# Kernel tuning notes

Hardware: AMD Instinct MI355X
Metric: run time of the kernel (lower is better)

The kernel has to match this reference:

```python
import math
import jax, jax.numpy as jnp
import numpy as np

H = 16  # num_heads
B, L, D = 1, 256, 1024


def setup_inputs() -> dict:
    key = jax.random.key(0)
    ks = jax.random.split(key, 12)
    s = 1.0 / math.sqrt(D)  # keep activations O(1)
    inp = {
        "mu": jax.random.normal(ks[0], (B, L, D), jnp.float32),
        "var": jax.random.uniform(ks[1], (B, L, D), jnp.float32) + 0.1,
    }
    names = ["q_mu", "q_var", "k_mu", "k_var", "v_mu", "v_var", "o_mu", "o_var"]
    for i, n in enumerate(names):
        inp["w" + n] = jax.random.normal(ks[2 + i], (D, D), jnp.float32) * s
        inp["b" + n] = jnp.zeros((D,), jnp.float32)
    return inp


def _split_heads(x):
    b, l, d = x.shape
    return x.reshape(b, l, H, d // H).transpose(0, 2, 1, 3)  # [B,H,L,Dh]


def _combine_heads(x):
    b, h, l, dh = x.shape
    return x.transpose(0, 2, 1, 3).reshape(b, l, h * dh)


def reference(mu, var, wq_mu, bq_mu, wq_var, bq_var, wk_mu, bk_mu, wk_var, bk_var,
              wv_mu, bv_mu, wv_var, bv_var, wo_mu, bo_mu, wo_var, bo_var):
    dk = mu.shape[-1] // H
    Qm = _split_heads(mu @ wq_mu + bq_mu)
    Qv = _split_heads(jax.nn.softplus(var @ wq_var + bq_var))
    Km = _split_heads(mu @ wk_mu + bk_mu)
    Kv = _split_heads(jax.nn.softplus(var @ wk_var + bk_var))
    Vm = _split_heads(mu @ wv_mu + bv_mu)
    Vv = _split_heads(jax.nn.softplus(var @ wv_var + bv_var))

    # per-element Gaussian KL, broadcast to [B,H,Lq,Lk,Dh] (as in the original)
    diff = (Qm[:, :, :, None, :] - Km[:, :, None, :, :]) ** 2
    ratio = Qv[:, :, :, None, :] / Kv[:, :, None, :, :]
    kl = diff / (2.0 * Kv[:, :, None, :, :]) + 0.5 * (ratio - jnp.log(ratio) - 1.0)
    scores = -kl.sum(-1) * (1.0 / math.sqrt(dk))  # [B,H,Lq,Lk]
    attn = jax.nn.softmax(scores, axis=-1)

    out_mu = jnp.einsum("bhqk,bhkd->bhqd", attn, Vm)
    out_var = jnp.einsum("bhqk,bhkd->bhqd", attn ** 2, Vv)

    O_mu = _combine_heads(out_mu)
    O_var = _combine_heads(out_var)
    mu_out = O_mu @ wo_mu + bo_mu
    var_out = jax.nn.softplus(O_var @ wo_var + bo_var)
    return mu_out, var_out
```

## Files before the change

### kernel.cpp

```cpp
#include <hip/hip_runtime.h>
#include <math.h>

typedef __bf16 bf16_t;
typedef bf16_t bf16x4 __attribute__((ext_vector_type(4)));
typedef bf16_t bf16x8 __attribute__((ext_vector_type(8)));
typedef float  f32x4  __attribute__((ext_vector_type(4)));

__device__ __forceinline__ float softplus_f(float x) {
    return (x > 20.f) ? x : log1pf(expf(x));
}

__device__ __forceinline__ float fast_rcp(float x) {
#if __has_builtin(__builtin_amdgcn_rcpf)
    return __builtin_amdgcn_rcpf(x);
#else
    return 1.0f / x;
#endif
}

template<bool AF32, int MT>
__device__ __forceinline__ void gemmT_core(const void* Aptr, const float* __restrict__ Wf,
                                           const int m_base, const int n_base,
                                           unsigned char* smem, const int t, f32x4* out) {
    constexpr int NA = 2 * MT;
    __syncthreads();
    bf16_t* stage = (bf16_t*)smem;
    float*  Cr    = (float*)smem;
    const int lane = t & 63, w = t >> 6;
    bf16_t* As = stage + w * 9216;
    bf16_t* Bs = As + 4608;
    const int r8 = lane >> 3, kb = lane & 7;
    const int fr = lane & 15, fq = lane >> 4, fk = fq * 8;
    const int bc = fr;
    const int br16 = fq * 16;

    const float*  Af = (const float*)Aptr  + (size_t)m_base * 1024 + w * 256 + kb * 8;
    const bf16_t* Ab = (const bf16_t*)Aptr + (size_t)m_base * 1024 + w * 256 + kb * 8;
    const float*  Bf = Wf + (size_t)(w * 256 + br16) * 1024 + n_base + bc * 4;

    f32x4 acc[MT][4] = {};
    bf16x8 pa[NA];
    f32x4 paf0[NA], paf1[NA];
    f32x4 pbf[16];

#pragma unroll
    for (int i = 0; i < NA; ++i) {
        if constexpr (AF32) {
            paf0[i] = *(const f32x4*)(Af + (size_t)(i * 8 + r8) * 1024);
            paf1[i] = *(const f32x4*)(Af + (size_t)(i * 8 + r8) * 1024 + 4);
        } else {
            pa[i] = *(const bf16x8*)(Ab + (size_t)(i * 8 + r8) * 1024);
        }
    }
#pragma unroll
    for (int i = 0; i < 16; ++i)
        pbf[i] = *(const f32x4*)(Bf + (size_t)i * 1024);

#pragma unroll
    for (int s = 0; s < 4; ++s) {
#pragma unroll
        for (int i = 0; i < NA; ++i) {
            bf16x8 av;
            if constexpr (AF32) {
#pragma unroll
                for (int e = 0; e < 4; ++e) {
                    av[e]     = (bf16_t)paf0[i][e];
                    av[e + 4] = (bf16_t)paf1[i][e];
                }
            } else {
                av = pa[i];
            }
            *(bf16x8*)&As[(i * 8 + r8) * 72 + kb * 8] = av;
        }
#pragma unroll
        for (int e = 0; e < 4; ++e) {
            bf16x8 lo, hi;
#pragma unroll
            for (int q = 0; q < 8; ++q) {
                lo[q] = (bf16_t)pbf[q][e];
                hi[q] = (bf16_t)pbf[q + 8][e];
            }
            *(bf16x8*)&Bs[(bc * 4 + e) * 72 + br16]     = lo;
            *(bf16x8*)&Bs[(bc * 4 + e) * 72 + br16 + 8] = hi;
        }
        if (s < 3) {
            const int off = (s + 1) * 64;
#pragma unroll
            for (int i = 0; i < NA; ++i) {
                if constexpr (AF32) {
                    paf0[i] = *(const f32x4*)(Af + (size_t)(i * 8 + r8) * 1024 + off);
                    paf1[i] = *(const f32x4*)(Af + (size_t)(i * 8 + r8) * 1024 + off + 4);
                } else {
                    pa[i] = *(const bf16x8*)(Ab + (size_t)(i * 8 + r8) * 1024 + off);
                }
            }
#pragma unroll
            for (int i = 0; i < 16; ++i)
                pbf[i] = *(const f32x4*)(Bf + (size_t)i * 1024 + (size_t)off * 1024);
        }
#pragma unroll
        for (int kh = 0; kh < 2; ++kh) {
            bf16x8 aF[MT], bF[4];
#pragma unroll
            for (int i = 0; i < MT; ++i)
                aF[i] = *(const bf16x8*)&As[(i * 16 + fr) * 72 + kh * 32 + fk];
#pragma unroll
            for (int j = 0; j < 4; ++j)
                bF[j] = *(const bf16x8*)&Bs[(j * 16 + fr) * 72 + kh * 32 + fk];
#pragma unroll
            for (int i = 0; i < MT; ++i)
#pragma unroll
                for (int j = 0; j < 4; ++j)
                    acc[i][j] = __builtin_amdgcn_mfma_f32_16x16x32_bf16(aF[i], bF[j], acc[i][j], 0, 0, 0);
        }
    }

    __syncthreads();
    {
        float* Crw = Cr + w * 4352;
        const int orow = fq * 4;
#pragma unroll
        for (int i = 0; i < MT; ++i)
#pragma unroll
            for (int j = 0; j < 4; ++j)
#pragma unroll
                for (int rr = 0; rr < 4; ++rr)
                    Crw[(i * 16 + orow + rr) * 68 + j * 16 + fr] = acc[i][j][rr];
    }
    __syncthreads();

    const int cc = (t & 15) * 4;
#pragma unroll
    for (int i = 0; i < MT; ++i) {
        const int row = (t >> 4) + i * 16;
        f32x4 s0 = *(const f32x4*)&Cr[0 * 4352 + row * 68 + cc];
        f32x4 s1 = *(const f32x4*)&Cr[1 * 4352 + row * 68 + cc];
        f32x4 s2 = *(const f32x4*)&Cr[2 * 4352 + row * 68 + cc];
        f32x4 s3 = *(const f32x4*)&Cr[3 * 4352 + row * 68 + cc];
        out[i] = (s0 + s1) + (s2 + s3);
    }
}

struct ProjArgs {
    const float* mu; const float* var;
    const float* W[6];
    const float* bias[6];
    float* Proj;
    bf16_t* Gbf; float* cvec;
};

__global__ __launch_bounds__(256, 2) void proj_kernel(ProjArgs a) {
    __shared__ __align__(16) unsigned char smem[73728];
    const int t = threadIdx.x;
    const int cc = (t & 15) * 4;
    const int L = blockIdx.x;
    const int x = L & 7;
    const int o = L >> 3;

    if (o < 32) {
        const int gA = (o >> 2) * 8 + x;
        const int m  = o & 3;
        const int zp = gA >> 4;
        const int nb = (gA & 15) * 64;
        const int mb = m * 64;
        const int wi = (zp < 2) ? zp : (zp + 2);
        const int sp = (zp == 1) || (zp == 3);
        const void* A = sp ? (const void*)a.var : (const void*)a.mu;
        f32x4 ov[4];
        gemmT_core<true, 4>(A, a.W[wi], mb, nb, smem, t, ov);
        const f32x4 bv = *(const f32x4*)&a.bias[wi][nb + cc];
        float* dst = a.Proj + (size_t)zp * 262144;
#pragma unroll
        for (int i = 0; i < 4; ++i) {
            const int row = (t >> 4) + i * 16;
            f32x4 v = ov[i] + bv;
            if (sp) {
                v[0] = softplus_f(v[0]); v[1] = softplus_f(v[1]);
                v[2] = softplus_f(v[2]); v[3] = softplus_f(v[3]);
            }
            *(f32x4*)&dst[(size_t)(mb + row) * 1024 + nb + cc] = v;
        }
    } else {
        const int op = o - 32;
        const int h  = (op >> 3) * 8 + x;
        const int m  = op & 7;
        const int mb = m * 32;
        const int nb = h * 64;
        f32x4 okm[2], okv[2];
        gemmT_core<true, 2>(a.mu,  a.W[2], mb, nb, smem, t, okm);
        gemmT_core<true, 2>(a.var, a.W[3], mb, nb, smem, t, okv);
        const f32x4 bkm = *(const f32x4*)&a.bias[2][nb + cc];
        const f32x4 bkv = *(const f32x4*)&a.bias[3][nb + cc];
#pragma unroll
        for (int i = 0; i < 2; ++i) {
            const int row = (t >> 4) + i * 16;
            const int katt = mb + row;
            const f32x4 km  = okm[i] + bkm;
            const f32x4 kvr = okv[i] + bkv;
            bf16x4 o1, o2;
            float c = 0.f;
#pragma unroll
            for (int e = 0; e < 4; ++e) {
                const float kv = softplus_f(kvr[e]);
                const float r  = 0.5f * fast_rcp(kv);
                o1[e] = (bf16_t)r;
                o2[e] = (bf16_t)(-2.f * km[e] * r);
                c += km[e] * km[e] * r + 0.5f * __logf(kv);
            }
            bf16_t* grow = a.Gbf + ((size_t)(h * 256 + katt)) * 128;
            *(bf16x4*)&grow[cc]      = o1;
            *(bf16x4*)&grow[64 + cc] = o2;
#pragma unroll
            for (int off = 8; off > 0; off >>= 1)
                c += __shfl_xor(c, off, 16);
            if ((t & 15) == 0)
                a.cvec[h * 256 + katt] = c;
        }
    }
}

#define OFF_VM   0
#define OFF_VV   36864
#define OFF_FS   73728
#define OFF_SC   82176
#define OFF_PHI  98816
#define OFF_PLO  107264
#define OFF_P2H  115712
#define OFF_P2L  124160
#define ATTN_SMEM 132608

__global__ __launch_bounds__(512) void attn_v7(const float* __restrict__ Qm,
                                               const float* __restrict__ Qv,
                                               const bf16_t* __restrict__ Gbf,
                                               const float* __restrict__ cvec,
                                               const float* __restrict__ Vm,
                                               const float* __restrict__ Vv,
                                               bf16_t* __restrict__ Omu,
                                               bf16_t* __restrict__ Ovar) {
    __shared__ __align__(16) unsigned char smem[ATTN_SMEM];
    bf16_t* Vsm = (bf16_t*)(smem + OFF_VM);
    bf16_t* Vsv = (bf16_t*)(smem + OFF_VV);
    float*  Fs  = (float*)(smem + OFF_FS);
    float*  Sc  = (float*)(smem + OFF_SC);
    bf16_t* Phi = (bf16_t*)(smem + OFF_PHI);
    bf16_t* Plo = (bf16_t*)(smem + OFF_PLO);
    bf16_t* P2h = (bf16_t*)(smem + OFF_P2H);
    bf16_t* P2l = (bf16_t*)(smem + OFF_P2L);

    const int L = blockIdx.x;
    const int h  = ((L >> 7) << 3) + (L & 7);
    const int qt = (L >> 3) & 15;

    const int t = threadIdx.x, w = t >> 6, lane = t & 63;
    const int fr = lane & 15, fq = lane >> 4;
    const int n0 = w * 32;

    const bf16_t* gB = Gbf + ((size_t)(h * 256 + n0 + fr)) * 128 + fq * 8;

    bf16x8 bcur[4];
#pragma unroll
    for (int ks = 0; ks < 4; ++ks) bcur[ks] = *(const bf16x8*)(gB + ks * 32);

    if (t < 256) {
        const int r = t >> 4, c = t & 15;
        f32x4 qm = *(const f32x4*)(Qm + (size_t)(qt * 16 + r) * 1024 + h * 64 + c * 4);
        f32x4 qv = *(const f32x4*)(Qv + (size_t)(qt * 16 + r) * 1024 + h * 64 + c * 4);
        *(f32x4*)&Fs[r * 132 + c * 4]      = qm * qm + qv;
        *(f32x4*)&Fs[r * 132 + 64 + c * 4] = qm;
    }
    __syncthreads();

    bf16x8 ahi[4], alo[4];
#pragma unroll
    for (int ks = 0; ks < 4; ++ks) {
        f32x4 f0 = *(const f32x4*)&Fs[fr * 132 + ks * 32 + fq * 8];
        f32x4 f1 = *(const f32x4*)&Fs[fr * 132 + ks * 32 + fq * 8 + 4];
#pragma unroll
        for (int e = 0; e < 4; ++e) {
            bf16_t hb = (bf16_t)f0[e];
            ahi[ks][e] = hb; alo[ks][e] = (bf16_t)(f0[e] - (float)hb);
            bf16_t hb2 = (bf16_t)f1[e];
            ahi[ks][e + 4] = hb2; alo[ks][e + 4] = (bf16_t)(f1[e] - (float)hb2);
        }
    }

    const int tm = t & 255;
    const int vk = tm >> 2, vpart = tm & 3;
    const float* Vsrc = (t >= 256) ? Vv : Vm;
    bf16_t*      Vdst = (t >= 256) ? Vsv : Vsm;

#pragma unroll
    for (int nt = 0; nt < 2; ++nt) {
        const int ra = vk + (2 * nt) * 64;
        const int rb = vk + (2 * nt + 1) * 64;
        const float* vsa = Vsrc + (size_t)ra * 1024 + h * 64 + vpart * 16;
        const float* vsb = Vsrc + (size_t)rb * 1024 + h * 64 + vpart * 16;
        f32x4 va0 = *(const f32x4*)(vsa),     va1 = *(const f32x4*)(vsa + 4);
        f32x4 va2 = *(const f32x4*)(vsa + 8), va3 = *(const f32x4*)(vsa + 12);
        f32x4 vb0 = *(const f32x4*)(vsb),     vb1 = *(const f32x4*)(vsb + 4);
        f32x4 vb2 = *(const f32x4*)(vsb + 8), vb3 = *(const f32x4*)(vsb + 12);

        bf16x8 bnxt[4];
        if (nt < 1) {
#pragma unroll
            for (int ks = 0; ks < 4; ++ks)
                bnxt[ks] = *(const bf16x8*)(gB + 2048 + ks * 32);
        }

        f32x4 acc = {0.f, 0.f, 0.f, 0.f};
#pragma unroll
        for (int ks = 0; ks < 4; ++ks) {
            acc = __builtin_amdgcn_mfma_f32_16x16x32_bf16(ahi[ks], bcur[ks], acc, 0, 0, 0);
            acc = __builtin_amdgcn_mfma_f32_16x16x32_bf16(alo[ks], bcur[ks], acc, 0, 0, 0);
        }

        {
            bf16_t* da = Vdst + ra * 72 + vpart * 16;
            bf16_t* db = Vdst + rb * 72 + vpart * 16;
            bf16x8 o0, o1;
            o0[0]=(bf16_t)va0[0]; o0[1]=(bf16_t)va0[1]; o0[2]=(bf16_t)va0[2]; o0[3]=(bf16_t)va0[3];
            o0[4]=(bf16_t)va1[0]; o0[5]=(bf16_t)va1[1]; o0[6]=(bf16_t)va1[2]; o0[7]=(bf16_t)va1[3];
            o1[0]=(bf16_t)va2[0]; o1[1]=(bf16_t)va2[1]; o1[2]=(bf16_t)va2[2]; o1[3]=(bf16_t)va2[3];
            o1[4]=(bf16_t)va3[0]; o1[5]=(bf16_t)va3[1]; o1[6]=(bf16_t)va3[2]; o1[7]=(bf16_t)va3[3];
            *(bf16x8*)(da)     = o0;
            *(bf16x8*)(da + 8) = o1;
            o0[0]=(bf16_t)vb0[0]; o0[1]=(bf16_t)vb0[1]; o0[2]=(bf16_t)vb0[2]; o0[3]=(bf16_t)vb0[3];
            o0[4]=(bf16_t)vb1[0]; o0[5]=(bf16_t)vb1[1]; o0[6]=(bf16_t)vb1[2]; o0[7]=(bf16_t)vb1[3];
            o1[0]=(bf16_t)vb2[0]; o1[1]=(bf16_t)vb2[1]; o1[2]=(bf16_t)vb2[2]; o1[3]=(bf16_t)vb2[3];
            o1[4]=(bf16_t)vb3[0]; o1[5]=(bf16_t)vb3[1]; o1[6]=(bf16_t)vb3[2]; o1[7]=(bf16_t)vb3[3];
            *(bf16x8*)(db)     = o0;
            *(bf16x8*)(db + 8) = o1;
        }

        const float cv = cvec[h * 256 + n0 + nt * 16 + fr];
        f32x4 lg = (acc + cv) * (-0.125f);
#pragma unroll
        for (int reg = 0; reg < 4; ++reg)
            Sc[(fq * 4 + reg) * 260 + n0 + nt * 16 + fr] = lg[reg];

#pragma unroll
        for (int ks = 0; ks < 4; ++ks) bcur[ks] = bnxt[ks];
    }
    __syncthreads();

    const int fw = w * 2;
    f32x4 sr[2];
#pragma unroll
    for (int r = 0; r < 2; ++r)
        sr[r] = *(const f32x4*)&Sc[(fw + r) * 260 + lane * 4];
#pragma unroll
    for (int r = 0; r < 2; ++r) {
        f32x4 s = sr[r];
        float mloc = fmaxf(fmaxf(s[0], s[1]), fmaxf(s[2], s[3]));
#pragma unroll
        for (int off = 32; off > 0; off >>= 1)
            mloc = fmaxf(mloc, __shfl_xor(mloc, off, 64));
        s[0] = __expf(s[0] - mloc); s[1] = __expf(s[1] - mloc);
        s[2] = __expf(s[2] - mloc); s[3] = __expf(s[3] - mloc);
        float sl = (s[0] + s[1]) + (s[2] + s[3]);
#pragma unroll
        for (int off = 32; off > 0; off >>= 1)
            sl += __shfl_xor(sl, off, 64);
        sr[r] = s * fast_rcp(sl);
    }

#pragma unroll
    for (int r = 0; r < 2; ++r) {
        bf16x4 phi, plo, p2hi, p2lo;
#pragma unroll
        for (int e = 0; e < 4; ++e) {
            const float p = sr[r][e];
            const bf16_t hb = (bf16_t)p;
            phi[e] = hb; plo[e] = (bf16_t)(p - (float)hb);
            const float p2 = p * p;
            const bf16_t h2 = (bf16_t)p2;
            p2hi[e] = h2; p2lo[e] = (bf16_t)(p2 - (float)h2);
        }
        const int row = fw + r;
        *(bf16x4*)&Phi[row * 264 + lane * 4] = phi;
        *(bf16x4*)&Plo[row * 264 + lane * 4] = plo;
        *(bf16x4*)&P2h[row * 264 + lane * 4] = p2hi;
        *(bf16x4*)&P2l[row * 264 + lane * 4] = p2lo;
    }
    __syncthreads();

    const int tile = w & 3;
    const int isvar = w >> 2;
    const bf16_t* Pa = isvar ? P2h : Phi;
    const bf16_t* Pb = isvar ? P2l : Plo;
    const bf16_t* Vs = isvar ? Vsv : Vsm;
    f32x4 accp = {0.f, 0.f, 0.f, 0.f};
#pragma unroll
    for (int k0 = 0; k0 < 256; k0 += 32) {
        const int ka = k0 + fq * 8;
        bf16x8 a1 = *(const bf16x8*)&Pa[fr * 264 + ka];
        bf16x8 a2 = *(const bf16x8*)&Pb[fr * 264 + ka];
        bf16x8 bfr;
#pragma unroll
        for (int j = 0; j < 8; ++j)
            bfr[j] = Vs[(ka + j) * 72 + tile * 16 + fr];
        accp = __builtin_amdgcn_mfma_f32_16x16x32_bf16(a1, bfr, accp, 0, 0, 0);
        accp = __builtin_amdgcn_mfma_f32_16x16x32_bf16(a2, bfr, accp, 0, 0, 0);
    }

    bf16_t* Out = isvar ? Ovar : Omu;
#pragma unroll
    for (int reg = 0; reg < 4; ++reg) {
        const int qg = qt * 16 + fq * 4 + reg;
        const size_t ob = (size_t)qg * 1024 + h * 64 + tile * 16 + fr;
        Out[ob] = (bf16_t)accp[reg];
    }
}

struct OutArgs {
    const bf16_t* A[2];
    const float*  W[2];
    const float*  bias[2];
    float*        dst[2];
    int           splus[2];
};

__global__ __launch_bounds__(256, 2) void out_gemm(OutArgs args) {
    __shared__ __align__(16) unsigned char smem[73728];
    const int t = threadIdx.x;
    const int L = blockIdx.x;
    const int x = L & 7, o = L >> 3;
    const int g = (o >> 2) * 8 + x;
    const int m = o & 3;
    const int z = g >> 4;
    const int n_base = (g & 15) * 64;
    const int m_base = m * 64;

    const bf16_t* __restrict__ A    = args.A[z];
    const float*  __restrict__ W    = args.W[z];
    const float*  __restrict__ bias = args.bias[z];
    float*        __restrict__ dst  = args.dst[z];
    const int sp = args.splus[z];

    f32x4 ov[4];
    gemmT_core<false, 4>(A, W, m_base, n_base, smem, t, ov);

    const int cc = (t & 15) * 4;
    const f32x4 bv = *(const f32x4*)&bias[n_base + cc];
#pragma unroll
    for (int i = 0; i < 4; ++i) {
        const int row = (t >> 4) + i * 16;
        f32x4 v = ov[i] + bv;
        if (sp) {
            v[0] = softplus_f(v[0]); v[1] = softplus_f(v[1]);
            v[2] = softplus_f(v[2]); v[3] = softplus_f(v[3]);
        }
        *(f32x4*)&dst[(size_t)(m_base + row) * 1024 + n_base + cc] = v;
    }
}

extern "C" void kernel_launch(void* const* d_in, const int* in_sizes, int n_in,
                              void* d_out, int out_size, void* d_ws, size_t ws_size,
                              hipStream_t stream) {
    const float* mu  = (const float*)d_in[0];
    const float* var = (const float*)d_in[1];
    uint8_t* ws = (uint8_t*)d_ws;

    float*  Proj = (float*)(ws);
    bf16_t* Obm  = (bf16_t*)(ws + (4u << 20));
    bf16_t* Obv  = (bf16_t*)(ws + (4u << 20) + (512u << 10));
    bf16_t* Gbf  = (bf16_t*)(ws + (5u << 20));
    float*  cvec = (float*)(ws + (6u << 20));

    ProjArgs pr;
    pr.mu = mu; pr.var = var;
    for (int i = 0; i < 6; ++i) {
        pr.W[i]    = (const float*)d_in[2 + 2 * i];
        pr.bias[i] = (const float*)d_in[3 + 2 * i];
    }
    pr.Proj = Proj; pr.Gbf = Gbf; pr.cvec = cvec;
    proj_kernel<<<dim3(384), 256, 0, stream>>>(pr);

    attn_v7<<<dim3(256), 512, 0, stream>>>(Proj, Proj + 262144, Gbf, cvec,
                                           Proj + 2 * 262144, Proj + 3 * 262144,
                                           Obm, Obv);

    OutArgs g3;
    g3.A[0] = Obm;  g3.W[0] = (const float*)d_in[14];
    g3.bias[0] = (const float*)d_in[15];
    g3.dst[0] = (float*)d_out;             g3.splus[0] = 0;
    g3.A[1] = Obv;  g3.W[1] = (const float*)d_in[16];
    g3.bias[1] = (const float*)d_in[17];
    g3.dst[1] = (float*)d_out + 262144;    g3.splus[1] = 1;
    out_gemm<<<dim3(128), 256, 0, stream>>>(g3);
}
```

Before: 144.5 us.

## Store V projections as head-major bf16 and fuse dual K GEMM

```diff
diff --git a/kernel.cpp b/kernel.cpp
--- a/kernel.cpp
+++ b/kernel.cpp
@@ -141,11 +141,126 @@
     }
 }
 
+__device__ __forceinline__ void gemmK_dual(const float* __restrict__ mu,
+                                           const float* __restrict__ var,
+                                           const float* __restrict__ Wkm,
+                                           const float* __restrict__ Wkv,
+                                           const int m_base, const int n_base,
+                                           unsigned char* smem, const int t,
+                                           f32x4 okm[2], f32x4 okv[2]) {
+    __syncthreads();
+    bf16_t* stage = (bf16_t*)smem;
+    float*  Cr    = (float*)smem;
+    const int lane = t & 63, w = t >> 6;
+    bf16_t* As = stage + w * 9216;
+    bf16_t* Bs = As + 4608;
+    const int r8 = lane >> 3, kb = lane & 7;
+    const int fr = lane & 15, fq = lane >> 4, fk = fq * 8;
+    const int bc = fr;
+    const int br16 = fq * 16;
+
+    const float* Asrc = (w < 2) ? mu : var;
+    const float* Wsrc = (w < 2) ? Wkm : Wkv;
+    const int kbase = (w & 1) * 512;
+
+    const float* Af = Asrc + (size_t)m_base * 1024 + kbase + kb * 8;
+    const float* Bf = Wsrc + (size_t)(kbase + br16) * 1024 + n_base + bc * 4;
+
+    f32x4 acc[2][4] = {};
+    f32x4 paf0[4], paf1[4];
+    f32x4 pbf[16];
+
+#pragma unroll
+    for (int i = 0; i < 4; ++i) {
+        paf0[i] = *(const f32x4*)(Af + (size_t)(i * 8 + r8) * 1024);
+        paf1[i] = *(const f32x4*)(Af + (size_t)(i * 8 + r8) * 1024 + 4);
+    }
+#pragma unroll
+    for (int i = 0; i < 16; ++i)
+        pbf[i] = *(const f32x4*)(Bf + (size_t)i * 1024);
+
+#pragma unroll
+    for (int s = 0; s < 8; ++s) {
+#pragma unroll
+        for (int i = 0; i < 4; ++i) {
+            bf16x8 av;
+#pragma unroll
+            for (int e = 0; e < 4; ++e) {
+                av[e]     = (bf16_t)paf0[i][e];
+                av[e + 4] = (bf16_t)paf1[i][e];
+            }
+            *(bf16x8*)&As[(i * 8 + r8) * 72 + kb * 8] = av;
+        }
+#pragma unroll
+        for (int e = 0; e < 4; ++e) {
+            bf16x8 lo, hi;
+#pragma unroll
+            for (int q = 0; q < 8; ++q) {
+                lo[q] = (bf16_t)pbf[q][e];
+                hi[q] = (bf16_t)pbf[q + 8][e];
+            }
+            *(bf16x8*)&Bs[(bc * 4 + e) * 72 + br16]     = lo;
+            *(bf16x8*)&Bs[(bc * 4 + e) * 72 + br16 + 8] = hi;
+        }
+        if (s < 7) {
+            const int off = (s + 1) * 64;
+#pragma unroll
+            for (int i = 0; i < 4; ++i) {
+                paf0[i] = *(const f32x4*)(Af + (size_t)(i * 8 + r8) * 1024 + off);
+                paf1[i] = *(const f32x4*)(Af + (size_t)(i * 8 + r8) * 1024 + off + 4);
+            }
+#pragma unroll
+            for (int i = 0; i < 16; ++i)
+                pbf[i] = *(const f32x4*)(Bf + (size_t)i * 1024 + (size_t)off * 1024);
+        }
+#pragma unroll
+        for (int kh = 0; kh < 2; ++kh) {
+            bf16x8 aF[2], bF[4];
+#pragma unroll
+            for (int i = 0; i < 2; ++i)
+                aF[i] = *(const bf16x8*)&As[(i * 16 + fr) * 72 + kh * 32 + fk];
+#pragma unroll
+            for (int j = 0; j < 4; ++j)
+                bF[j] = *(const bf16x8*)&Bs[(j * 16 + fr) * 72 + kh * 32 + fk];
+#pragma unroll
+            for (int i = 0; i < 2; ++i)
+#pragma unroll
+                for (int j = 0; j < 4; ++j)
+                    acc[i][j] = __builtin_amdgcn_mfma_f32_16x16x32_bf16(aF[i], bF[j], acc[i][j], 0, 0, 0);
+        }
+    }
+
+    __syncthreads();
+    {
+        float* Crw = Cr + w * 4352;
+        const int orow = fq * 4;
+#pragma unroll
+        for (int i = 0; i < 2; ++i)
+#pragma unroll
+            for (int j = 0; j < 4; ++j)
+#pragma unroll
+                for (int rr = 0; rr < 4; ++rr)
+                    Crw[(i * 16 + orow + rr) * 68 + j * 16 + fr] = acc[i][j][rr];
+    }
+    __syncthreads();
+
+    const int cc = (t & 15) * 4;
+#pragma unroll
+    for (int i = 0; i < 2; ++i) {
+        const int row = (t >> 4) + i * 16;
+        okm[i] = *(const f32x4*)&Cr[0 * 4352 + row * 68 + cc]
+               + *(const f32x4*)&Cr[1 * 4352 + row * 68 + cc];
+        okv[i] = *(const f32x4*)&Cr[2 * 4352 + row * 68 + cc]
+               + *(const f32x4*)&Cr[3 * 4352 + row * 68 + cc];
+    }
+}
+
 struct ProjArgs {
     const float* mu; const float* var;
     const float* W[6];
     const float* bias[6];
     float* Proj;
+    bf16_t* Vbm; bf16_t* Vbv;
     bf16_t* Gbf; float* cvec;
 };
 
@@ -169,16 +284,33 @@
         f32x4 ov[4];
         gemmT_core<true, 4>(A, a.W[wi], mb, nb, smem, t, ov);
         const f32x4 bv = *(const f32x4*)&a.bias[wi][nb + cc];
-        float* dst = a.Proj + (size_t)zp * 262144;
-#pragma unroll
-        for (int i = 0; i < 4; ++i) {
-            const int row = (t >> 4) + i * 16;
-            f32x4 v = ov[i] + bv;
-            if (sp) {
-                v[0] = softplus_f(v[0]); v[1] = softplus_f(v[1]);
-                v[2] = softplus_f(v[2]); v[3] = softplus_f(v[3]);
-            }
-            *(f32x4*)&dst[(size_t)(mb + row) * 1024 + nb + cc] = v;
+        if (zp < 2) {
+            float* dst = a.Proj + (size_t)zp * 262144;
+#pragma unroll
+            for (int i = 0; i < 4; ++i) {
+                const int row = (t >> 4) + i * 16;
+                f32x4 v = ov[i] + bv;
+                if (sp) {
+                    v[0] = softplus_f(v[0]); v[1] = softplus_f(v[1]);
+                    v[2] = softplus_f(v[2]); v[3] = softplus_f(v[3]);
+                }
+                *(f32x4*)&dst[(size_t)(mb + row) * 1024 + nb + cc] = v;
+            }
+        } else {
+            bf16_t* dst = ((zp == 2) ? a.Vbm : a.Vbv) + (size_t)(nb >> 6) * 16384;
+#pragma unroll
+            for (int i = 0; i < 4; ++i) {
+                const int row = (t >> 4) + i * 16;
+                f32x4 v = ov[i] + bv;
+                if (sp) {
+                    v[0] = softplus_f(v[0]); v[1] = softplus_f(v[1]);
+                    v[2] = softplus_f(v[2]); v[3] = softplus_f(v[3]);
+                }
+                bf16x4 o4;
+                o4[0] = (bf16_t)v[0]; o4[1] = (bf16_t)v[1];
+                o4[2] = (bf16_t)v[2]; o4[3] = (bf16_t)v[3];
+                *(bf16x4*)&dst[(size_t)(mb + row) * 64 + cc] = o4;
+            }
         }
     } else {
         const int op = o - 32;
@@ -187,8 +319,7 @@
         const int mb = m * 32;
         const int nb = h * 64;
         f32x4 okm[2], okv[2];
-        gemmT_core<true, 2>(a.mu,  a.W[2], mb, nb, smem, t, okm);
-        gemmT_core<true, 2>(a.var, a.W[3], mb, nb, smem, t, okv);
+        gemmK_dual(a.mu, a.var, a.W[2], a.W[3], mb, nb, smem, t, okm, okv);
         const f32x4 bkm = *(const f32x4*)&a.bias[2][nb + cc];
         const f32x4 bkv = *(const f32x4*)&a.bias[3][nb + cc];
 #pragma unroll
@@ -233,8 +364,8 @@
                                                const float* __restrict__ Qv,
                                                const bf16_t* __restrict__ Gbf,
                                                const float* __restrict__ cvec,
-                                               const float* __restrict__ Vm,
-                                               const float* __restrict__ Vv,
+                                               const bf16_t* __restrict__ Vbm,
+                                               const bf16_t* __restrict__ Vbv,
                                                bf16_t* __restrict__ Omu,
                                                bf16_t* __restrict__ Ovar) {
     __shared__ __align__(16) unsigned char smem[ATTN_SMEM];
@@ -286,19 +417,17 @@
 
     const int tm = t & 255;
     const int vk = tm >> 2, vpart = tm & 3;
-    const float* Vsrc = (t >= 256) ? Vv : Vm;
+    const bf16_t* Vsrc = ((t >= 256) ? Vbv : Vbm) + (size_t)h * 16384;
     bf16_t*      Vdst = (t >= 256) ? Vsv : Vsm;
 
 #pragma unroll
     for (int nt = 0; nt < 2; ++nt) {
         const int ra = vk + (2 * nt) * 64;
         const int rb = vk + (2 * nt + 1) * 64;
-        const float* vsa = Vsrc + (size_t)ra * 1024 + h * 64 + vpart * 16;
-        const float* vsb = Vsrc + (size_t)rb * 1024 + h * 64 + vpart * 16;
-        f32x4 va0 = *(const f32x4*)(vsa),     va1 = *(const f32x4*)(vsa + 4);
-        f32x4 va2 = *(const f32x4*)(vsa + 8), va3 = *(const f32x4*)(vsa + 12);
-        f32x4 vb0 = *(const f32x4*)(vsb),     vb1 = *(const f32x4*)(vsb + 4);
-        f32x4 vb2 = *(const f32x4*)(vsb + 8), vb3 = *(const f32x4*)(vsb + 12);
+        bf16x8 pa0 = *(const bf16x8*)(Vsrc + (size_t)ra * 64 + vpart * 16);
+        bf16x8 pa1 = *(const bf16x8*)(Vsrc + (size_t)ra * 64 + vpart * 16 + 8);
+        bf16x8 pb0 = *(const bf16x8*)(Vsrc + (size_t)rb * 64 + vpart * 16);
+        bf16x8 pb1 = *(const bf16x8*)(Vsrc + (size_t)rb * 64 + vpart * 16 + 8);
 
         bf16x8 bnxt[4];
         if (nt < 1) {
@@ -317,19 +446,10 @@
         {
             bf16_t* da = Vdst + ra * 72 + vpart * 16;
             bf16_t* db = Vdst + rb * 72 + vpart * 16;
-            bf16x8 o0, o1;
-            o0[0]=(bf16_t)va0[0]; o0[1]=(bf16_t)va0[1]; o0[2]=(bf16_t)va0[2]; o0[3]=(bf16_t)va0[3];
-            o0[4]=(bf16_t)va1[0]; o0[5]=(bf16_t)va1[1]; o0[6]=(bf16_t)va1[2]; o0[7]=(bf16_t)va1[3];
-            o1[0]=(bf16_t)va2[0]; o1[1]=(bf16_t)va2[1]; o1[2]=(bf16_t)va2[2]; o1[3]=(bf16_t)va2[3];
-            o1[4]=(bf16_t)va3[0]; o1[5]=(bf16_t)va3[1]; o1[6]=(bf16_t)va3[2]; o1[7]=(bf16_t)va3[3];
-            *(bf16x8*)(da)     = o0;
-            *(bf16x8*)(da + 8) = o1;
-            o0[0]=(bf16_t)vb0[0]; o0[1]=(bf16_t)vb0[1]; o0[2]=(bf16_t)vb0[2]; o0[3]=(bf16_t)vb0[3];
-            o0[4]=(bf16_t)vb1[0]; o0[5]=(bf16_t)vb1[1]; o0[6]=(bf16_t)vb1[2]; o0[7]=(bf16_t)vb1[3];
-            o1[0]=(bf16_t)vb2[0]; o1[1]=(bf16_t)vb2[1]; o1[2]=(bf16_t)vb2[2]; o1[3]=(bf16_t)vb2[3];
-            o1[4]=(bf16_t)vb3[0]; o1[5]=(bf16_t)vb3[1]; o1[6]=(bf16_t)vb3[2]; o1[7]=(bf16_t)vb3[3];
-            *(bf16x8*)(db)     = o0;
-            *(bf16x8*)(db + 8) = o1;
+            *(bf16x8*)(da)     = pa0;
+            *(bf16x8*)(da + 8) = pa1;
+            *(bf16x8*)(db)     = pb0;
+            *(bf16x8*)(db + 8) = pb1;
         }
 
         const float cv = cvec[h * 256 + n0 + nt * 16 + fr];
@@ -462,10 +582,12 @@
     uint8_t* ws = (uint8_t*)d_ws;
 
     float*  Proj = (float*)(ws);
-    bf16_t* Obm  = (bf16_t*)(ws + (4u << 20));
-    bf16_t* Obv  = (bf16_t*)(ws + (4u << 20) + (512u << 10));
-    bf16_t* Gbf  = (bf16_t*)(ws + (5u << 20));
-    float*  cvec = (float*)(ws + (6u << 20));
+    bf16_t* Vbm  = (bf16_t*)(ws + (2u << 20));
+    bf16_t* Vbv  = (bf16_t*)(ws + (2u << 20) + (512u << 10));
+    bf16_t* Obm  = (bf16_t*)(ws + (3u << 20));
+    bf16_t* Obv  = (bf16_t*)(ws + (3u << 20) + (512u << 10));
+    bf16_t* Gbf  = (bf16_t*)(ws + (4u << 20));
+    float*  cvec = (float*)(ws + (5u << 20));
 
     ProjArgs pr;
     pr.mu = mu; pr.var = var;
@@ -473,12 +595,11 @@
         pr.W[i]    = (const float*)d_in[2 + 2 * i];
         pr.bias[i] = (const float*)d_in[3 + 2 * i];
     }
-    pr.Proj = Proj; pr.Gbf = Gbf; pr.cvec = cvec;
+    pr.Proj = Proj; pr.Vbm = Vbm; pr.Vbv = Vbv; pr.Gbf = Gbf; pr.cvec = cvec;
     proj_kernel<<<dim3(384), 256, 0, stream>>>(pr);
 
     attn_v7<<<dim3(256), 512, 0, stream>>>(Proj, Proj + 262144, Gbf, cvec,
-                                           Proj + 2 * 262144, Proj + 3 * 262144,
-                                           Obm, Obv);
+                                           Vbm, Vbv, Obm, Obv);
 
     OutArgs g3;
     g3.A[0] = Obm;  g3.W[0] = (const float*)d_in[14];
```

Result: no change. 142.7 us (-1.2%).
